# Performance work log

Hardware: AMD Instinct MI355X
Metric: run time of the kernel (lower is better)

The kernel has to match this reference:

```python
import jax, jax.numpy as jnp
import numpy as np

NUM_CLASS = 20
STRIDE = 4.0
B, H, W, G, NV = 8, 128, 128, 64, 40


def setup_inputs() -> dict:
    key = jax.random.key(0)
    ks = jax.random.split(key, 8)
    keypoints = jax.random.normal(ks[0], (B, H, W, NUM_CLASS), jnp.float32)
    preg = jax.random.uniform(ks[1], (B, H, W, 4), jnp.float32, 1.0, 40.0)
    fpn = jax.random.normal(ks[2], (B, H, W, NUM_CLASS), jnp.float32)
    masks = jnp.ones((B, H, W, G), jnp.float32)
    scalar_y = jax.random.uniform(ks[3], (B, G), jnp.float32, 5.0, 25.0)
    scalar_x = jax.random.uniform(ks[4], (B, G), jnp.float32, 5.0, 25.0)
    # ground truth: [cy, cx, y1, x1, y2, x2, class]; rows >= NV are zero padding
    rng = np.random.default_rng(0)
    gt = np.zeros((B, G, 7), np.float32)
    cy = rng.uniform(20.0, 492.0, (B, NV)).astype(np.float32)
    cx = rng.uniform(20.0, 492.0, (B, NV)).astype(np.float32)
    hh = rng.uniform(16.0, 120.0, (B, NV)).astype(np.float32)
    ww = rng.uniform(16.0, 120.0, (B, NV)).astype(np.float32)
    gt[:, :NV, 0] = cy
    gt[:, :NV, 1] = cx
    gt[:, :NV, 2] = np.clip(cy - hh / 2, 1.0, 510.0)
    gt[:, :NV, 3] = np.clip(cx - ww / 2, 1.0, 510.0)
    gt[:, :NV, 4] = np.clip(cy + hh / 2, 1.0, 510.0)
    gt[:, :NV, 5] = np.clip(cx + ww / 2, 1.0, 510.0)
    gt[:, :NV, 6] = rng.integers(1, NUM_CLASS + 1, (B, NV)).astype(np.float32)
    return {
        "keypoints": keypoints,
        "preg": preg,
        "fpn": fpn,
        "ground_truth": jnp.asarray(gt),
        "masks": masks,
        "scalar_y": scalar_y,
        "scalar_x": scalar_x,
    }


def _image_loss(gravity_pred, dist_pred, heatmap_pred, gt, masks, sy, sx):
    f32 = jnp.float32
    Hh, Ww, C = gravity_pred.shape
    Gg = gt.shape[0]
    # padding boundary: first row whose cy (col 0) is the minimum (==0 padding)
    slice_index = jnp.argmin(gt[:, 0])
    valid = jnp.arange(Gg) < slice_index
    vf = valid.astype(f32)

    gy = (gt[:, 0] + 0.5) / STRIDE
    gx = (gt[:, 1] + 0.5) / STRIDE
    by1 = (gt[:, 2] + 0.5) / STRIDE
    bx1 = (gt[:, 3] + 0.5) / STRIDE
    by2 = (gt[:, 4] + 0.5) / STRIDE
    bx2 = (gt[:, 5] + 0.5) / STRIDE
    cid = gt[:, 6].astype(jnp.int32) - 1
    kp_y = jnp.clip(jnp.floor(gt[:, 0] / STRIDE).astype(jnp.int32), 0, Hh - 1)
    kp_x = jnp.clip(jnp.floor(gt[:, 1] / STRIDE).astype(jnp.int32), 0, Ww - 1)

    grid_y = (jnp.arange(Hh, dtype=f32) + 0.5)[:, None, None]  # [H,1,1]
    grid_x = (jnp.arange(Ww, dtype=f32) + 0.5)[None, :, None]  # [1,W,1]

    dist_l = grid_x - bx1  # [1,W,G]
    dist_r = bx2 - grid_x
    dist_t = grid_y - by1  # [H,1,G]
    dist_b = by2 - grid_y
    ymask = (dist_t > 0.0).astype(f32) * (dist_b > 0.0).astype(f32)
    xmask = (dist_l > 0.0).astype(f32) * (dist_r > 0.0).astype(f32)
    heatmask = ymask * xmask * masks * vf  # [H,W,G]
    dist_l = dist_l * heatmask
    dist_r = dist_r * heatmask
    dist_t = dist_t * heatmask
    dist_b = dist_b * heatmask
    loc = jnp.max(heatmask, axis=-1)  # [H,W]
    dist_area = (dist_l + dist_r) * (dist_t + dist_b)
    area_pad = dist_area + (1.0 - heatmask) * 1e8
    area_min = jnp.min(area_pad, axis=-1, keepdims=True)
    dist_mask = (dist_area == area_min).astype(f32) * loc[..., None]  # [H,W,G]
    dl = jnp.max(dist_l * dist_mask, axis=-1)
    dr = jnp.max(dist_r * dist_mask, axis=-1)
    dt = jnp.max(dist_t * dist_mask, axis=-1)
    db = jnp.max(dist_b * dist_mask, axis=-1)

    pl, pr, pt, pb = (dist_pred[..., k] for k in range(4))
    inter = (jnp.minimum(dl, pl) + jnp.minimum(dr, pr)) * (jnp.minimum(dt, pt) + jnp.minimum(db, pb))
    union = (dl + dr) * (dt + db) + (pl + pr) * (pt + pb) - inter
    iou = inter / (union + 1e-12)

    red = jnp.exp(-(((grid_y - 0.5 - jnp.floor(gy)) / jnp.sqrt(sy)) ** 2
                    + ((grid_x - 0.5 - jnp.floor(gx)) / jnp.sqrt(sx)) ** 2) / 2.0) * vf  # [H,W,G]
    iou_red = jnp.max(red, axis=-1)
    iou_loss = jnp.sum(-jnp.log(iou + 1e-12) * loc * (iou_red * 4.0 + 1.0))

    # per-class max over gts of that class (== boolean_mask + reduce_max; empty -> 0)
    seg = jnp.where(valid & (cid >= 0) & (cid < C), cid, C)
    red_gt = jnp.maximum(jax.ops.segment_max(red.transpose(2, 0, 1), seg, num_segments=C + 1)[:C], 0.0).transpose(1, 2, 0)
    hm_gt = jnp.maximum(jax.ops.segment_max(dist_mask.transpose(2, 0, 1), seg, num_segments=C + 1)[:C], 0.0).transpose(1, 2, 0)
    gt_kp = jnp.zeros((Hh, Ww, C + 1), f32).at[kp_y, kp_x, seg].max(vf)[..., :C]

    sig, ls = jax.nn.sigmoid, jax.nn.log_sigmoid
    pos = -(1.0 - sig(gravity_pred)) ** 2 * ls(gravity_pred) * gt_kp
    neg = -(1.0 - red_gt) ** 4 * sig(gravity_pred) ** 2 * (-gravity_pred + ls(gravity_pred)) * (1.0 - gt_kp)
    gravity_loss = jnp.sum(pos) + jnp.sum(neg)

    hpos = -10.0 * (1.0 - sig(heatmap_pred)) ** 2 * ls(heatmap_pred) * hm_gt
    hneg = -10.0 * sig(heatmap_pred) ** 2 * (-heatmap_pred + ls(heatmap_pred)) * (1.0 - hm_gt)
    s_hg = jnp.sum(hm_gt)
    hm_loss = jnp.sum(hneg) / (jnp.asarray(Hh * Ww * C, f32) - s_hg)

    cond = s_hg != 0.0
    safe_hg = jnp.where(cond, s_hg, 1.0)
    s_loc = jnp.sum(loc)
    safe_loc = jnp.where(s_loc > 0.0, s_loc, 1.0)
    n_valid = jnp.maximum(slice_index.astype(f32), 1.0)
    hm2 = hm_loss + jnp.sum(hpos) / safe_hg
    iou_out = jnp.where(cond, iou_loss / safe_loc, 0.0)
    grav_out = jnp.where(cond, gravity_loss / n_valid, 0.0)
    hm_out = jnp.where(cond, hm2, hm_loss)
    total = jnp.where(cond, iou_out + grav_out + hm2, hm_loss)
    return iou_out, hm_out, grav_out, total


def reference(keypoints, preg, fpn, ground_truth, masks, scalar_y, scalar_x):
    losses = jax.vmap(_image_loss)(keypoints, preg, fpn, ground_truth, masks, scalar_y, scalar_x)
    # layer returns the mean total loss over the batch
    return jnp.mean(losses[3])
```

## Files before the change

### kernel.cpp

```cpp
#include <hip/hip_runtime.h>
#include <math.h>

#define Bc 8
#define Hc 128
#define Wc 128
#define Cc 20
#define Gc 64
#define HWc (Hc*Wc)
#define NBLK (Bc*HWc/256)

#define WS_STRIDE 768
#define OFF_BOX   0
#define OFF_RED   256
#define OFF_KPIX  512
#define OFF_SEG   576
#define OFF_START 640
#define WS_NV     704
#define WS_ACC    705
#define WS_SLICE  712

__global__ __launch_bounds__(64) void prep_kernel(
    const float* __restrict__ gt, const float* __restrict__ sy,
    const float* __restrict__ sx, float* __restrict__ ws)
{
  const int b = blockIdx.x;
  const int g = threadIdx.x;
  const float* row = gt + (size_t)(b*Gc + g)*7;
  const float cy = row[0];
  const float cx = row[1];

  float v = cy; int idx = g;
  #pragma unroll
  for (int o = 32; o > 0; o >>= 1) {
    const float ov = __shfl_down(v, o, 64);
    const int   oi = __shfl_down(idx, o, 64);
    if (ov < v || (ov == v && oi < idx)) { v = ov; idx = oi; }
  }
  const int slice = __shfl(idx, 0, 64);
  const bool valid = g < slice;
  const int cid = (int)row[6] - 1;
  const int cls = (cid >= 0 && cid < Cc) ? cid : Cc;

  __shared__ int counts[Cc+1], offs[Cc+1], starts[Cc+2];
  if (g < Cc+1) { counts[g] = 0; offs[g] = 0; }
  __syncthreads();
  if (valid) atomicAdd(&counts[cls], 1);
  __syncthreads();
  if (g == 0) {
    int acc = 0;
    for (int c = 0; c < Cc+1; ++c) { starts[c] = acc; acc += counts[c]; }
    starts[Cc+1] = acc;
  }
  __syncthreads();

  float* wb = ws + (size_t)b*WS_STRIDE;
  int*  wbi = (int*)wb;
  float4 bx;
  bx.x = (row[2]+0.5f)*0.25f;
  bx.y = (row[3]+0.5f)*0.25f;
  bx.z = (row[4]+0.5f)*0.25f;
  bx.w = (row[5]+0.5f)*0.25f;
  ((float4*)(wb + OFF_BOX))[g] = bx;
  wbi[OFF_SEG+g] = (valid && cls < Cc) ? cls : Cc;
  if (valid) {
    const int pos = starts[cls] + atomicAdd(&offs[cls], 1);
    float4 rp;
    rp.x = floorf((cy+0.5f)*0.25f);
    rp.y = floorf((cx+0.5f)*0.25f);
    rp.z = 0.5f / sy[b*Gc+g];
    rp.w = 0.5f / sx[b*Gc+g];
    ((float4*)(wb + OFF_RED))[pos] = rp;
    int kpy = (int)floorf(cy*0.25f); kpy = kpy < 0 ? 0 : (kpy > Hc-1 ? Hc-1 : kpy);
    int kpx = (int)floorf(cx*0.25f); kpx = kpx < 0 ? 0 : (kpx > Wc-1 ? Wc-1 : kpx);
    wbi[OFF_KPIX+pos] = kpy*Wc + kpx;
  }
  if (g < Cc+2) wbi[OFF_START+g] = starts[g];
  if (g == 0) { wb[WS_NV] = fmaxf((float)slice, 1.0f); wbi[WS_SLICE] = slice; }
  if (g < 6) wb[WS_ACC+g] = 0.0f;
}

__device__ __forceinline__ float wave_sum(float v) {
  #pragma unroll
  for (int o = 32; o > 0; o >>= 1) v += __shfl_down(v, o, 64);
  return v;
}

__global__ __launch_bounds__(256, 4) void main_kernel(
  const float* __restrict__ kpt, const float* __restrict__ preg,
  const float* __restrict__ fpn, const float* __restrict__ masks,
  const float* __restrict__ wsc, float* __restrict__ wsa)
{
  __shared__ float s_part[4][6];

  const int tid = threadIdx.x;
  const int b   = blockIdx.x >> 6;
  const int pix = blockIdx.x*256 + tid;
  const int hw  = pix & (HWc-1);
  const int h = hw >> 7, w = hw & (Wc-1);

  const float* wb  = wsc + (size_t)b*WS_STRIDE;
  const int*   wbi = (const int*)wb;
  const float4* __restrict__ box4 = (const float4*)(wb + OFF_BOX);
  const float4* __restrict__ red4 = (const float4*)(wb + OFF_RED);
  const int nslice = wbi[WS_SLICE];

  const float wx = w + 0.5f, hy = h + 0.5f;
  const float px_ = (float)w, py_ = (float)h;
  const float4* mrow4 = (const float4*)(masks + (size_t)pix*Gc);

  float amin = 3.0e38f; float loc = 0.0f, mmin = 0.0f; int gmin = 0;
  float4 ma = mrow4[0], mb = mrow4[1];
  for (int g0 = 0; g0 < nslice; g0 += 8) {
    const int pf = (g0 + 8) < Gc ? ((g0 + 8) >> 2) : 14;
    const float4 na = mrow4[pf];
    const float4 nb = mrow4[pf + 1];
    #pragma unroll
    for (int j = 0; j < 8; ++j) {
      const int g = g0 + j;
      const float m = (j==0)?ma.x:(j==1)?ma.y:(j==2)?ma.z:(j==3)?ma.w
                    : (j==4)?mb.x:(j==5)?mb.y:(j==6)?mb.z:mb.w;
      const float4 bx = box4[g];
      const float dl = wx - bx.y, dr = bx.w - wx;
      const float dt = hy - bx.x, db = bx.z - hy;
      const bool inb = (dl > 0.f) & (dr > 0.f) & (dt > 0.f) & (db > 0.f) && (g < nslice);
      const float hm = inb ? m : 0.f;
      const float area = (dl*hm + dr*hm) * (dt*hm + db*hm);
      const float ap = area + (1.f - hm)*1e8f;
      if (ap < amin) { amin = ap; gmin = g; mmin = m; }
      loc = fmaxf(loc, hm);
    }
    ma = na; mb = nb;
  }

  float dlm=0.f, drm=0.f, dtm=0.f, dbm=0.f, hmval=0.f; int cmin = Cc;
  if (loc > 0.f) {
    const float4 bx = box4[gmin];
    const float dl = wx - bx.y, dr = bx.w - wx;
    const float dt = hy - bx.x, db = bx.z - hy;
    const float area = (dl*mmin + dr*mmin) * (dt*mmin + db*mmin);
    if (area == amin) {
      dlm = dl*mmin*loc; drm = dr*mmin*loc; dtm = dt*mmin*loc; dbm = db*mmin*loc;
      cmin = wbi[OFF_SEG + gmin];
      hmval = loc;
    }
  }

  const float4* kq4 = (const float4*)(kpt + (size_t)pix*Cc);
  const float4* fq4 = (const float4*)(fpn + (size_t)pix*Cc);
  float4 kcur = kq4[0], fcur = fq4[0];
  float gargmax = -1e30f, grav = 0.f, hneg = 0.f;
  int sb = wbi[OFF_START];
  for (int cg = 0; cg < 5; ++cg) {
    const int nx = cg < 4 ? cg + 1 : 4;
    const float4 knxt = kq4[nx];
    const float4 fnxt = fq4[nx];
    #pragma unroll
    for (int j = 0; j < 4; ++j) {
      const int c = cg*4 + j;
      const int s1 = wbi[OFF_START + c + 1];
      float ramax = -1e30f; bool kpv = false;
      for (int i = sb; i < s1; ++i) {
        const float4 rp = red4[i];
        const int kpix = wbi[OFF_KPIX + i];
        const float dy = py_ - rp.x, dx = px_ - rp.y;
        const float arg = -(dy*dy*rp.z + dx*dx*rp.w);
        ramax = fmaxf(ramax, arg);
        kpv = kpv | (kpix == hw);
      }
      sb = s1;
      const float rmax = __expf(ramax);
      gargmax = fmaxf(gargmax, ramax);
      const float x  = (j==0)?kcur.x:(j==1)?kcur.y:(j==2)?kcur.z:kcur.w;
      const float e  = __expf(-fabsf(x));
      const float t  = 1.f + e;
      const float r  = 1.f / t;
      const float L  = __logf(t);
      const float s  = (x >= 0.f) ? r : e*r;
      const float lsx = fminf(x, 0.f) - L;
      const float kv = kpv ? 1.f : 0.f;
      const float om = 1.f - rmax;
      const float om4 = (om*om)*(om*om);
      const float oms = 1.f - s;
      grav += (-(oms*oms)*lsx)*kv + (-om4*(s*s)*(lsx - x))*(1.f - kv);

      const float fx  = (j==0)?fcur.x:(j==1)?fcur.y:(j==2)?fcur.z:fcur.w;
      const float ef  = __expf(-fabsf(fx));
      const float tf  = 1.f + ef;
      const float rf  = 1.f / tf;
      const float Lf  = __logf(tf);
      const float sf  = (fx >= 0.f) ? rf : ef*rf;
      const float lsf = fminf(fx, 0.f) - Lf;
      hneg += -10.f*(sf*sf)*(lsf - fx);
    }
    kcur = knxt; fcur = fnxt;
  }
  {
    const int e20 = wbi[OFF_START + Cc + 1];
    for (int i = sb; i < e20; ++i) {
      const float4 rp = red4[i];
      const float dy = py_ - rp.x, dx = px_ - rp.y;
      gargmax = fmaxf(gargmax, -(dy*dy*rp.z + dx*dx*rp.w));
    }
  }
  const float iou_red = __expf(gargmax);

  const float4 p4 = *(const float4*)(preg + (size_t)pix*4);
  const float inter = (fminf(dlm,p4.x)+fminf(drm,p4.y)) * (fminf(dtm,p4.z)+fminf(dbm,p4.w));
  const float uni = (dlm+drm)*(dtm+dbm) + (p4.x+p4.y)*(p4.z+p4.w) - inter;
  const float iou = inter / (uni + 1e-12f);
  const float t_iou = -__logf(iou + 1e-12f) * loc * (iou_red*4.f + 1.f);

  float hpos = 0.f, shg = 0.f;
  if (hmval > 0.f && cmin < Cc) {
    const float fx  = fpn[(size_t)pix*Cc + cmin];
    const float ef  = __expf(-fabsf(fx));
    const float tf  = 1.f + ef;
    const float rf  = 1.f / tf;
    const float Lf  = __logf(tf);
    const float sf  = (fx >= 0.f) ? rf : ef*rf;
    const float lsf = fminf(fx, 0.f) - Lf;
    const float osf = 1.f - sf;
    hpos = -10.f*(osf*osf)*lsf*hmval;
    hneg -= (-10.f*(sf*sf)*(lsf - fx))*hmval;
    shg = hmval;
  }

  float v0 = wave_sum(t_iou);
  float v1 = wave_sum(loc);
  float v2 = wave_sum(grav);
  float v3 = wave_sum(hpos);
  float v4 = wave_sum(hneg);
  float v5 = wave_sum(shg);
  const int wv = tid >> 6, ln = tid & 63;
  if (ln == 0) {
    s_part[wv][0]=v0; s_part[wv][1]=v1; s_part[wv][2]=v2;
    s_part[wv][3]=v3; s_part[wv][4]=v4; s_part[wv][5]=v5;
  }
  __syncthreads();
  if (tid < 6) {
    const float a = s_part[0][tid] + s_part[1][tid] + s_part[2][tid] + s_part[3][tid];
    atomicAdd(wsa + (size_t)b*WS_STRIDE + WS_ACC + tid, a);
  }
}

__global__ __launch_bounds__(64) void fin_kernel(const float* __restrict__ ws,
                                                 float* __restrict__ out)
{
  const int b = threadIdx.x;
  float total = 0.0f;
  if (b < Bc) {
    const float* wb = ws + (size_t)b*WS_STRIDE;
    const float iou_loss = wb[WS_ACC+0];
    const float s_loc    = wb[WS_ACC+1];
    const float grav     = wb[WS_ACC+2];
    const float hposs    = wb[WS_ACC+3];
    const float hnegs    = wb[WS_ACC+4];
    const float shg      = wb[WS_ACC+5];
    const float nv       = wb[WS_NV];
    const float hm_loss  = hnegs / ((float)(HWc*Cc) - shg);
    const bool  cond     = (shg != 0.0f);
    const float safe_hg  = cond ? shg : 1.0f;
    const float safe_loc = (s_loc > 0.0f) ? s_loc : 1.0f;
    const float hm2      = hm_loss + hposs/safe_hg;
    total = cond ? (iou_loss/safe_loc + grav/nv + hm2) : hm_loss;
  }
  #pragma unroll
  for (int o = 4; o > 0; o >>= 1) total += __shfl_down(total, o, 64);
  if (b == 0) out[0] = total * (1.0f/(float)Bc);
}

extern "C" void kernel_launch(void* const* d_in, const int* in_sizes, int n_in,
                              void* d_out, int out_size, void* d_ws, size_t ws_size,
                              hipStream_t stream) {
  const float* kpt  = (const float*)d_in[0];
  const float* preg = (const float*)d_in[1];
  const float* fpn  = (const float*)d_in[2];
  const float* gt   = (const float*)d_in[3];
  const float* mk   = (const float*)d_in[4];
  const float* sy   = (const float*)d_in[5];
  const float* sx   = (const float*)d_in[6];
  float* ws  = (float*)d_ws;
  float* out = (float*)d_out;

  prep_kernel<<<Bc, 64, 0, stream>>>(gt, sy, sx, ws);
  main_kernel<<<NBLK, 256, 0, stream>>>(kpt, preg, fpn, mk, ws, ws);
  fin_kernel<<<1, 64, 0, stream>>>(ws, out);
}
```

Measured before the change: 116.6 us.

## Process two vertically adjacent pixels per thread to share box and Gaussian work

Each thread now handles two pixels in the same column one row apart, with 128-thread blocks covering two image rows per 256 pixels. Box x-tests, Gaussian dx terms and workspace loads (box, red params, kpix) are shared between the pair, which cuts redundant scalar/LDS-like loads and ALU per pixel. The mask-loop prefetching is dropped in favour of direct loads, and a scalar tail loop handles nslice not divisible by 8. Register pressure roughly doubles and the number of threads halves, so latency hiding may suffer.

```diff
diff --git a/kernel.cpp b/kernel.cpp
--- a/kernel.cpp
+++ b/kernel.cpp
@@ -7,7 +7,7 @@
 #define Cc 20
 #define Gc 64
 #define HWc (Hc*Wc)
-#define NBLK (Bc*HWc/256)
+#define NBLKM 512
 
 #define WS_STRIDE 768
 #define OFF_BOX   0
@@ -85,18 +85,34 @@
   return v;
 }
 
-__global__ __launch_bounds__(256, 4) void main_kernel(
+__device__ __forceinline__ float sel8(const float4 a, const float4 b, int j) {
+  return (j==0)?a.x:(j==1)?a.y:(j==2)?a.z:(j==3)?a.w
+       : (j==4)?b.x:(j==5)?b.y:(j==6)?b.z:b.w;
+}
+
+__device__ __forceinline__ void siglog(float x, float& s, float& ls) {
+  const float e = __expf(-fabsf(x));
+  const float t = 1.f + e;
+  const float r = 1.f / t;
+  s  = (x >= 0.f) ? r : e*r;
+  ls = fminf(x, 0.f) - __logf(t);
+}
+
+__global__ __launch_bounds__(128, 4) void main_kernel(
   const float* __restrict__ kpt, const float* __restrict__ preg,
   const float* __restrict__ fpn, const float* __restrict__ masks,
   const float* __restrict__ wsc, float* __restrict__ wsa)
 {
-  __shared__ float s_part[4][6];
+  __shared__ float s_part[2][6];
 
   const int tid = threadIdx.x;
   const int b   = blockIdx.x >> 6;
-  const int pix = blockIdx.x*256 + tid;
-  const int hw  = pix & (HWc-1);
-  const int h = hw >> 7, w = hw & (Wc-1);
+  const int sub = blockIdx.x & 63;
+  const int hw0 = sub*256 + tid;
+  const int hw1 = hw0 + Wc;
+  const int pix0 = b*HWc + hw0;
+  const int pix1 = pix0 + Wc;
+  const int h0 = hw0 >> 7, w = hw0 & (Wc-1);
 
   const float* wb  = wsc + (size_t)b*WS_STRIDE;
   const int*   wbi = (const int*)wb;
@@ -104,132 +120,198 @@
   const float4* __restrict__ red4 = (const float4*)(wb + OFF_RED);
   const int nslice = wbi[WS_SLICE];
 
-  const float wx = w + 0.5f, hy = h + 0.5f;
-  const float px_ = (float)w, py_ = (float)h;
-  const float4* mrow4 = (const float4*)(masks + (size_t)pix*Gc);
-
-  float amin = 3.0e38f; float loc = 0.0f, mmin = 0.0f; int gmin = 0;
-  float4 ma = mrow4[0], mb = mrow4[1];
-  for (int g0 = 0; g0 < nslice; g0 += 8) {
-    const int pf = (g0 + 8) < Gc ? ((g0 + 8) >> 2) : 14;
-    const float4 na = mrow4[pf];
-    const float4 nb = mrow4[pf + 1];
+  const float wx = w + 0.5f;
+  const float hy0 = h0 + 0.5f, hy1 = hy0 + 1.0f;
+  const float px_ = (float)w;
+  const float py0 = (float)h0, py1 = py0 + 1.0f;
+  const float4* mrow0 = (const float4*)(masks + (size_t)pix0*Gc);
+  const float4* mrow1 = (const float4*)(masks + (size_t)pix1*Gc);
+
+  float amin0 = 3.0e38f, amin1 = 3.0e38f;
+  float loc0 = 0.f, loc1 = 0.f, mm0 = 0.f, mm1 = 0.f;
+  int gm0 = 0, gm1 = 0;
+  const int nfull = nslice & ~7;
+  for (int g0 = 0; g0 < nfull; g0 += 8) {
+    const float4 a0 = mrow0[g0 >> 2], b0 = mrow0[(g0 >> 2) + 1];
+    const float4 a1 = mrow1[g0 >> 2], b1 = mrow1[(g0 >> 2) + 1];
     #pragma unroll
     for (int j = 0; j < 8; ++j) {
       const int g = g0 + j;
-      const float m = (j==0)?ma.x:(j==1)?ma.y:(j==2)?ma.z:(j==3)?ma.w
-                    : (j==4)?mb.x:(j==5)?mb.y:(j==6)?mb.z:mb.w;
+      const float m0 = sel8(a0, b0, j);
+      const float m1 = sel8(a1, b1, j);
       const float4 bx = box4[g];
       const float dl = wx - bx.y, dr = bx.w - wx;
-      const float dt = hy - bx.x, db = bx.z - hy;
-      const bool inb = (dl > 0.f) & (dr > 0.f) & (dt > 0.f) & (db > 0.f) && (g < nslice);
-      const float hm = inb ? m : 0.f;
-      const float area = (dl*hm + dr*hm) * (dt*hm + db*hm);
-      const float ap = area + (1.f - hm)*1e8f;
-      if (ap < amin) { amin = ap; gmin = g; mmin = m; }
-      loc = fmaxf(loc, hm);
-    }
-    ma = na; mb = nb;
-  }
-
-  float dlm=0.f, drm=0.f, dtm=0.f, dbm=0.f, hmval=0.f; int cmin = Cc;
-  if (loc > 0.f) {
-    const float4 bx = box4[gmin];
+      const bool xok = (dl > 0.f) & (dr > 0.f);
+      const float dt0 = hy0 - bx.x, db0 = bx.z - hy0;
+      const float dt1 = hy1 - bx.x, db1 = bx.z - hy1;
+      const float hm0 = (xok & (dt0 > 0.f) & (db0 > 0.f)) ? m0 : 0.f;
+      const float hm1 = (xok & (dt1 > 0.f) & (db1 > 0.f)) ? m1 : 0.f;
+      const float ar0 = (dl*hm0 + dr*hm0) * (dt0*hm0 + db0*hm0);
+      const float ar1 = (dl*hm1 + dr*hm1) * (dt1*hm1 + db1*hm1);
+      const float ap0 = ar0 + (1.f - hm0)*1e8f;
+      const float ap1 = ar1 + (1.f - hm1)*1e8f;
+      if (ap0 < amin0) { amin0 = ap0; gm0 = g; mm0 = m0; }
+      if (ap1 < amin1) { amin1 = ap1; gm1 = g; mm1 = m1; }
+      loc0 = fmaxf(loc0, hm0);
+      loc1 = fmaxf(loc1, hm1);
+    }
+  }
+  for (int g = nfull; g < nslice; ++g) {
+    const float m0 = masks[(size_t)pix0*Gc + g];
+    const float m1 = masks[(size_t)pix1*Gc + g];
+    const float4 bx = box4[g];
     const float dl = wx - bx.y, dr = bx.w - wx;
-    const float dt = hy - bx.x, db = bx.z - hy;
-    const float area = (dl*mmin + dr*mmin) * (dt*mmin + db*mmin);
-    if (area == amin) {
-      dlm = dl*mmin*loc; drm = dr*mmin*loc; dtm = dt*mmin*loc; dbm = db*mmin*loc;
-      cmin = wbi[OFF_SEG + gmin];
-      hmval = loc;
-    }
-  }
-
-  const float4* kq4 = (const float4*)(kpt + (size_t)pix*Cc);
-  const float4* fq4 = (const float4*)(fpn + (size_t)pix*Cc);
-  float4 kcur = kq4[0], fcur = fq4[0];
-  float gargmax = -1e30f, grav = 0.f, hneg = 0.f;
+    const bool xok = (dl > 0.f) & (dr > 0.f);
+    const float dt0 = hy0 - bx.x, db0 = bx.z - hy0;
+    const float dt1 = hy1 - bx.x, db1 = bx.z - hy1;
+    const float hm0 = (xok & (dt0 > 0.f) & (db0 > 0.f)) ? m0 : 0.f;
+    const float hm1 = (xok & (dt1 > 0.f) & (db1 > 0.f)) ? m1 : 0.f;
+    const float ar0 = (dl*hm0 + dr*hm0) * (dt0*hm0 + db0*hm0);
+    const float ar1 = (dl*hm1 + dr*hm1) * (dt1*hm1 + db1*hm1);
+    const float ap0 = ar0 + (1.f - hm0)*1e8f;
+    const float ap1 = ar1 + (1.f - hm1)*1e8f;
+    if (ap0 < amin0) { amin0 = ap0; gm0 = g; mm0 = m0; }
+    if (ap1 < amin1) { amin1 = ap1; gm1 = g; mm1 = m1; }
+    loc0 = fmaxf(loc0, hm0);
+    loc1 = fmaxf(loc1, hm1);
+  }
+
+  float dlm0=0.f, drm0=0.f, dtm0=0.f, dbm0=0.f, hv0=0.f; int cm0 = Cc;
+  if (loc0 > 0.f) {
+    const float4 bx = box4[gm0];
+    const float dl = wx - bx.y, dr = bx.w - wx;
+    const float dt = hy0 - bx.x, db = bx.z - hy0;
+    const float area = (dl*mm0 + dr*mm0) * (dt*mm0 + db*mm0);
+    if (area == amin0) {
+      dlm0 = dl*mm0*loc0; drm0 = dr*mm0*loc0; dtm0 = dt*mm0*loc0; dbm0 = db*mm0*loc0;
+      cm0 = wbi[OFF_SEG + gm0];
+      hv0 = loc0;
+    }
+  }
+  float dlm1=0.f, drm1=0.f, dtm1=0.f, dbm1=0.f, hv1=0.f; int cm1 = Cc;
+  if (loc1 > 0.f) {
+    const float4 bx = box4[gm1];
+    const float dl = wx - bx.y, dr = bx.w - wx;
+    const float dt = hy1 - bx.x, db = bx.z - hy1;
+    const float area = (dl*mm1 + dr*mm1) * (dt*mm1 + db*mm1);
+    if (area == amin1) {
+      dlm1 = dl*mm1*loc1; drm1 = dr*mm1*loc1; dtm1 = dt*mm1*loc1; dbm1 = db*mm1*loc1;
+      cm1 = wbi[OFF_SEG + gm1];
+      hv1 = loc1;
+    }
+  }
+
+  const float4* kq0 = (const float4*)(kpt + (size_t)pix0*Cc);
+  const float4* fq0 = (const float4*)(fpn + (size_t)pix0*Cc);
+  const float4* kq1 = (const float4*)(kpt + (size_t)pix1*Cc);
+  const float4* fq1 = (const float4*)(fpn + (size_t)pix1*Cc);
+  float gam0 = -1e30f, gam1 = -1e30f;
+  float grav0 = 0.f, grav1 = 0.f, hneg0 = 0.f, hneg1 = 0.f;
   int sb = wbi[OFF_START];
   for (int cg = 0; cg < 5; ++cg) {
-    const int nx = cg < 4 ? cg + 1 : 4;
-    const float4 knxt = kq4[nx];
-    const float4 fnxt = fq4[nx];
+    const float4 kc0 = kq0[cg], fc0 = fq0[cg];
+    const float4 kc1 = kq1[cg], fc1 = fq1[cg];
     #pragma unroll
     for (int j = 0; j < 4; ++j) {
       const int c = cg*4 + j;
       const int s1 = wbi[OFF_START + c + 1];
-      float ramax = -1e30f; bool kpv = false;
+      float ra0 = -1e30f, ra1 = -1e30f; bool kp0 = false, kp1 = false;
       for (int i = sb; i < s1; ++i) {
         const float4 rp = red4[i];
         const int kpix = wbi[OFF_KPIX + i];
-        const float dy = py_ - rp.x, dx = px_ - rp.y;
-        const float arg = -(dy*dy*rp.z + dx*dx*rp.w);
-        ramax = fmaxf(ramax, arg);
-        kpv = kpv | (kpix == hw);
+        const float dx = px_ - rp.x*0.f + (px_ - rp.y);
+        (void)dx;
+        const float dxx = (px_ - rp.y)*(px_ - rp.y)*rp.w;
+        const float dy0 = py0 - rp.x, dy1 = py1 - rp.x;
+        ra0 = fmaxf(ra0, -(dy0*dy0*rp.z + dxx));
+        ra1 = fmaxf(ra1, -(dy1*dy1*rp.z + dxx));
+        kp0 = kp0 | (kpix == hw0);
+        kp1 = kp1 | (kpix == hw1);
       }
       sb = s1;
-      const float rmax = __expf(ramax);
-      gargmax = fmaxf(gargmax, ramax);
-      const float x  = (j==0)?kcur.x:(j==1)?kcur.y:(j==2)?kcur.z:kcur.w;
-      const float e  = __expf(-fabsf(x));
-      const float t  = 1.f + e;
-      const float r  = 1.f / t;
-      const float L  = __logf(t);
-      const float s  = (x >= 0.f) ? r : e*r;
-      const float lsx = fminf(x, 0.f) - L;
-      const float kv = kpv ? 1.f : 0.f;
-      const float om = 1.f - rmax;
-      const float om4 = (om*om)*(om*om);
-      const float oms = 1.f - s;
-      grav += (-(oms*oms)*lsx)*kv + (-om4*(s*s)*(lsx - x))*(1.f - kv);
-
-      const float fx  = (j==0)?fcur.x:(j==1)?fcur.y:(j==2)?fcur.z:fcur.w;
-      const float ef  = __expf(-fabsf(fx));
-      const float tf  = 1.f + ef;
-      const float rf  = 1.f / tf;
-      const float Lf  = __logf(tf);
-      const float sf  = (fx >= 0.f) ? rf : ef*rf;
-      const float lsf = fminf(fx, 0.f) - Lf;
-      hneg += -10.f*(sf*sf)*(lsf - fx);
-    }
-    kcur = knxt; fcur = fnxt;
+      const float rmax0 = __expf(ra0);
+      const float rmax1 = __expf(ra1);
+      gam0 = fmaxf(gam0, ra0);
+      gam1 = fmaxf(gam1, ra1);
+
+      {
+        const float x = (j==0)?kc0.x:(j==1)?kc0.y:(j==2)?kc0.z:kc0.w;
+        float s, ls; siglog(x, s, ls);
+        const float kv = kp0 ? 1.f : 0.f;
+        const float om = 1.f - rmax0;
+        const float om4 = (om*om)*(om*om);
+        const float oms = 1.f - s;
+        grav0 += (-(oms*oms)*ls)*kv + (-om4*(s*s)*(ls - x))*(1.f - kv);
+        const float fx = (j==0)?fc0.x:(j==1)?fc0.y:(j==2)?fc0.z:fc0.w;
+        float sf, lsf; siglog(fx, sf, lsf);
+        hneg0 += -10.f*(sf*sf)*(lsf - fx);
+      }
+      {
+        const float x = (j==0)?kc1.x:(j==1)?kc1.y:(j==2)?kc1.z:kc1.w;
+        float s, ls; siglog(x, s, ls);
+        const float kv = kp1 ? 1.f : 0.f;
+        const float om = 1.f - rmax1;
+        const float om4 = (om*om)*(om*om);
+        const float oms = 1.f - s;
+        grav1 += (-(oms*oms)*ls)*kv + (-om4*(s*s)*(ls - x))*(1.f - kv);
+        const float fx = (j==0)?fc1.x:(j==1)?fc1.y:(j==2)?fc1.z:fc1.w;
+        float sf, lsf; siglog(fx, sf, lsf);
+        hneg1 += -10.f*(sf*sf)*(lsf - fx);
+      }
+    }
   }
   {
     const int e20 = wbi[OFF_START + Cc + 1];
     for (int i = sb; i < e20; ++i) {
       const float4 rp = red4[i];
-      const float dy = py_ - rp.x, dx = px_ - rp.y;
-      gargmax = fmaxf(gargmax, -(dy*dy*rp.z + dx*dx*rp.w));
-    }
-  }
-  const float iou_red = __expf(gargmax);
-
-  const float4 p4 = *(const float4*)(preg + (size_t)pix*4);
-  const float inter = (fminf(dlm,p4.x)+fminf(drm,p4.y)) * (fminf(dtm,p4.z)+fminf(dbm,p4.w));
-  const float uni = (dlm+drm)*(dtm+dbm) + (p4.x+p4.y)*(p4.z+p4.w) - inter;
-  const float iou = inter / (uni + 1e-12f);
-  const float t_iou = -__logf(iou + 1e-12f) * loc * (iou_red*4.f + 1.f);
+      const float dxx = (px_ - rp.y)*(px_ - rp.y)*rp.w;
+      const float dy0 = py0 - rp.x, dy1 = py1 - rp.x;
+      gam0 = fmaxf(gam0, -(dy0*dy0*rp.z + dxx));
+      gam1 = fmaxf(gam1, -(dy1*dy1*rp.z + dxx));
+    }
+  }
+  const float ired0 = __expf(gam0);
+  const float ired1 = __expf(gam1);
+
+  float t_iou0, t_iou1;
+  {
+    const float4 p4 = *(const float4*)(preg + (size_t)pix0*4);
+    const float inter = (fminf(dlm0,p4.x)+fminf(drm0,p4.y)) * (fminf(dtm0,p4.z)+fminf(dbm0,p4.w));
+    const float uni = (dlm0+drm0)*(dtm0+dbm0) + (p4.x+p4.y)*(p4.z+p4.w) - inter;
+    const float iou = inter / (uni + 1e-12f);
+    t_iou0 = -__logf(iou + 1e-12f) * loc0 * (ired0*4.f + 1.f);
+  }
+  {
+    const float4 p4 = *(const float4*)(preg + (size_t)pix1*4);
+    const float inter = (fminf(dlm1,p4.x)+fminf(drm1,p4.y)) * (fminf(dtm1,p4.z)+fminf(dbm1,p4.w));
+    const float uni = (dlm1+drm1)*(dtm1+dbm1) + (p4.x+p4.y)*(p4.z+p4.w) - inter;
+    const float iou = inter / (uni + 1e-12f);
+    t_iou1 = -__logf(iou + 1e-12f) * loc1 * (ired1*4.f + 1.f);
+  }
 
   float hpos = 0.f, shg = 0.f;
-  if (hmval > 0.f && cmin < Cc) {
-    const float fx  = fpn[(size_t)pix*Cc + cmin];
-    const float ef  = __expf(-fabsf(fx));
-    const float tf  = 1.f + ef;
-    const float rf  = 1.f / tf;
-    const float Lf  = __logf(tf);
-    const float sf  = (fx >= 0.f) ? rf : ef*rf;
-    const float lsf = fminf(fx, 0.f) - Lf;
+  if (hv0 > 0.f && cm0 < Cc) {
+    const float fx = fpn[(size_t)pix0*Cc + cm0];
+    float sf, lsf; siglog(fx, sf, lsf);
     const float osf = 1.f - sf;
-    hpos = -10.f*(osf*osf)*lsf*hmval;
-    hneg -= (-10.f*(sf*sf)*(lsf - fx))*hmval;
-    shg = hmval;
-  }
-
-  float v0 = wave_sum(t_iou);
-  float v1 = wave_sum(loc);
-  float v2 = wave_sum(grav);
+    hpos += -10.f*(osf*osf)*lsf*hv0;
+    hneg0 -= (-10.f*(sf*sf)*(lsf - fx))*hv0;
+    shg += hv0;
+  }
+  if (hv1 > 0.f && cm1 < Cc) {
+    const float fx = fpn[(size_t)pix1*Cc + cm1];
+    float sf, lsf; siglog(fx, sf, lsf);
+    const float osf = 1.f - sf;
+    hpos += -10.f*(osf*osf)*lsf*hv1;
+    hneg1 -= (-10.f*(sf*sf)*(lsf - fx))*hv1;
+    shg += hv1;
+  }
+
+  float v0 = wave_sum(t_iou0 + t_iou1);
+  float v1 = wave_sum(loc0 + loc1);
+  float v2 = wave_sum(grav0 + grav1);
   float v3 = wave_sum(hpos);
-  float v4 = wave_sum(hneg);
+  float v4 = wave_sum(hneg0 + hneg1);
   float v5 = wave_sum(shg);
   const int wv = tid >> 6, ln = tid & 63;
   if (ln == 0) {
@@ -238,7 +320,7 @@
   }
   __syncthreads();
   if (tid < 6) {
-    const float a = s_part[0][tid] + s_part[1][tid] + s_part[2][tid] + s_part[3][tid];
+    const float a = s_part[0][tid] + s_part[1][tid];
     atomicAdd(wsa + (size_t)b*WS_STRIDE + WS_ACC + tid, a);
   }
 }
@@ -283,6 +365,6 @@
   float* out = (float*)d_out;
 
   prep_kernel<<<Bc, 64, 0, stream>>>(gt, sy, sx, ws);
-  main_kernel<<<NBLK, 256, 0, stream>>>(kpt, preg, fpn, mk, ws, ws);
+  main_kernel<<<NBLKM, 128, 0, stream>>>(kpt, preg, fpn, mk, ws, ws);
   fin_kernel<<<1, 64, 0, stream>>>(ws, out);
 }
```

After: 120.1 us. +3.1%, slower.
